# Performance work log

Measured on AMD Instinct MI355X. Metric: run time of the kernel, lower is better.

Reference implementation:

```python
import jax, jax.numpy as jnp
import numpy as np

N = 1_000_000          # total nodes (atoms)
F = 32                 # node feature dim
K = 16                 # kernels per degree
DEG_COUNTS = [200_000, 300_000, 300_000, 200_000]  # focal nodes per degree 1..4
EPS = 1e-8


def _unit(a):
    # L2-normalize along last axis (CosineSimilarity semantics)
    return a / (jnp.linalg.norm(a, axis=-1, keepdims=True) + EPS)


def setup_inputs() -> dict:
    key = jax.random.key(0)
    ks = jax.random.split(key, 16)
    x = jax.random.normal(ks[0], (N, F), dtype=jnp.float32)
    # selected indices: disjoint partition of all nodes by degree (a permutation)
    perm = jax.random.permutation(ks[1], N)
    sels, off = [], 0
    for c in DEG_COUNTS:
        sels.append(perm[off:off + c].astype(jnp.int64))
        off += c
    inp = {"x": x}
    for d in range(1, 5):
        inp[f"selected_index_deg{d}"] = sels[d - 1]
        inp[f"nei_index_deg{d}"] = jax.random.randint(
            ks[1 + d], (d * DEG_COUNTS[d - 1],), 0, N).astype(jnp.int64)
        inp[f"W_focal{d}"] = jax.random.normal(ks[7 + d], (K, F), dtype=jnp.float32)
        inp[f"W_nei{d}"] = jax.random.normal(ks[11 + d], (K, d, F), dtype=jnp.float32)
    return inp


def _degree_score(x, sel, nei, Wf, Wn, deg):
    # gather receptive field for this degree group
    x_focal = _unit(x[sel])                         # (Nd, F)
    x_nei = _unit(x[nei].reshape(-1, deg, F))       # (Nd, deg, F)
    sc_f = _unit(Wf) @ x_focal.T                    # (K, Nd) cosine vs focal kernel
    sc_n = jnp.einsum('kdf,ndf->kn', _unit(Wn), x_nei) / deg  # mean neighbor cosine
    return sc_f + sc_n                              # (K, Nd)


def reference(x,
              W_focal1, W_nei1, W_focal2, W_nei2,
              W_focal3, W_nei3, W_focal4, W_nei4,
              selected_index_deg1, selected_index_deg2,
              selected_index_deg3, selected_index_deg4,
              nei_index_deg1, nei_index_deg2,
              nei_index_deg3, nei_index_deg4):
    sels = [selected_index_deg1, selected_index_deg2,
            selected_index_deg3, selected_index_deg4]
    neis = [nei_index_deg1, nei_index_deg2, nei_index_deg3, nei_index_deg4]
    Wfs = [W_focal1, W_focal2, W_focal3, W_focal4]
    Wns = [W_nei1, W_nei2, W_nei3, W_nei4]

    out = jnp.zeros((4 * K, N), dtype=x.dtype)  # the `zeros` score matrix
    row, col = 0, 0
    for d in range(1, 5):
        sc = _degree_score(x, sels[d - 1], neis[d - 1], Wfs[d - 1], Wns[d - 1], d)
        nd = sels[d - 1].shape[0]
        out = out.at[row:row + K, col:col + nd].set(sc)
        row += K
        col += nd
    # reorder columns back to original node order (get_reorder_index -> sort)
    order = jnp.argsort(jnp.concatenate(sels))
    return out[:, order].T  # (N, 4*K)
```

## Files before the change

### kernel.cpp

```cpp
#include <hip/hip_runtime.h>
#include <math.h>

#define F 32
#define K 16
#define EPSN 1e-8f
#define NPB 512


typedef _Float16 half8 __attribute__((ext_vector_type(8)));
typedef float f32x4  __attribute__((ext_vector_type(4)));
typedef int   i32x2  __attribute__((ext_vector_type(2)));
typedef int   i32x4  __attribute__((ext_vector_type(4)));

#define VMWAIT(N) do { asm volatile("s_waitcnt vmcnt(%0)" :: "n"(N) : "memory"); \
                       __builtin_amdgcn_sched_barrier(0); } while (0)

__device__ __forceinline__ void gpair(f32x4& a, f32x4& b, const float* x,
                                      unsigned row, int kq) {
    const unsigned off = row * 128u + (unsigned)kq * 32u;
    asm volatile("global_load_dwordx4 %0, %1, %2"
                 : "=&v"(a) : "v"(off), "s"(x) : "memory");
    asm volatile("global_load_dwordx4 %0, %1, %2 offset:16"
                 : "=&v"(b) : "v"(off), "s"(x) : "memory");
}

__device__ __forceinline__ void gstore(float* out, unsigned off, f32x4 v) {
    asm volatile("global_store_dwordx4 %0, %1, %2"
                 :: "v"(off), "v"(v), "s"(out) : "memory");
}

template<int DEG> struct Idx;
template<> struct Idx<1> { int node; int n0;
    __device__ __forceinline__ int nb(int) const { return n0; } };
template<> struct Idx<2> { int node; i32x2 nn;
    __device__ __forceinline__ int nb(int j) const { return nn[j]; } };
template<> struct Idx<3> { int node; i32x2 nn; int n2;
    __device__ __forceinline__ int nb(int j) const { return j < 2 ? nn[j] : n2; } };
template<> struct Idx<4> { int node; i32x4 nn;
    __device__ __forceinline__ int nb(int j) const { return nn[j]; } };

template<int DEG>
__device__ __forceinline__ void load_idx(Idx<DEG>& d, const int* sel,
                                         const int* nei, int ic) {
    const unsigned so = (unsigned)ic << 2;
    asm volatile("global_load_dword %0, %1, %2"
                 : "=&v"(d.node) : "v"(so), "s"(sel) : "memory");
    const unsigned no = (unsigned)(ic * DEG) << 2;
    if constexpr (DEG == 1)
        asm volatile("global_load_dword %0, %1, %2"
                     : "=&v"(d.n0) : "v"(no), "s"(nei) : "memory");
    else if constexpr (DEG == 2)
        asm volatile("global_load_dwordx2 %0, %1, %2"
                     : "=&v"(d.nn) : "v"(no), "s"(nei) : "memory");
    else if constexpr (DEG == 3) {
        asm volatile("global_load_dwordx2 %0, %1, %2"
                     : "=&v"(d.nn) : "v"(no), "s"(nei) : "memory");
        asm volatile("global_load_dword %0, %1, %2 offset:8"
                     : "=&v"(d.n2) : "v"(no), "s"(nei) : "memory");
    } else
        asm volatile("global_load_dwordx4 %0, %1, %2"
                     : "=&v"(d.nn) : "v"(no), "s"(nei) : "memory");
}

template<int DEG>
__device__ __forceinline__ f32x4 slab_compute(f32x4 a, f32x4 b, f32x4 acc,
                                              const _Float16* sWh,
                                              const _Float16* sWl,
                                              int lane, int r) {
    float ss = a[0]*a[0] + a[1]*a[1] + a[2]*a[2] + a[3]*a[3]
             + b[0]*b[0] + b[1]*b[1] + b[2]*b[2] + b[3]*b[3];
    ss += __shfl_xor(ss, 16);
    ss += __shfl_xor(ss, 32);
    float sc = 1.f / (sqrtf(ss) + EPSN);
    if (r > 0) sc *= (1.f / (float)DEG);
    const float f0 = a[0]*sc, f1 = a[1]*sc, f2 = a[2]*sc, f3 = a[3]*sc;
    const float f4 = b[0]*sc, f5 = b[1]*sc, f6 = b[2]*sc, f7 = b[3]*sc;
    half8 bh, bl;
    bh[0]=(_Float16)f0; bl[0]=(_Float16)(f0-(float)bh[0]);
    bh[1]=(_Float16)f1; bl[1]=(_Float16)(f1-(float)bh[1]);
    bh[2]=(_Float16)f2; bl[2]=(_Float16)(f2-(float)bh[2]);
    bh[3]=(_Float16)f3; bl[3]=(_Float16)(f3-(float)bh[3]);
    bh[4]=(_Float16)f4; bl[4]=(_Float16)(f4-(float)bh[4]);
    bh[5]=(_Float16)f5; bl[5]=(_Float16)(f5-(float)bh[5]);
    bh[6]=(_Float16)f6; bl[6]=(_Float16)(f6-(float)bh[6]);
    bh[7]=(_Float16)f7; bl[7]=(_Float16)(f7-(float)bh[7]);
    const int aoff = r * 512 + lane * 8;
    const half8 ah = *(const half8*)(sWh + aoff);
    const half8 al = *(const half8*)(sWl + aoff);
    acc = __builtin_amdgcn_mfma_f32_16x16x32_f16(ah, bh, acc, 0, 0, 0);
    acc = __builtin_amdgcn_mfma_f32_16x16x32_f16(ah, bl, acc, 0, 0, 0);
    acc = __builtin_amdgcn_mfma_f32_16x16x32_f16(al, bh, acc, 0, 0, 0);
    return acc;
}

template<int DEG>
__device__ __forceinline__ void process_deg(const float* __restrict__ x,
                                            const int*   __restrict__ sel,
                                            const int*   __restrict__ nei,
                                            const float* __restrict__ Wf,
                                            const float* __restrict__ Wn,
                                            float* __restrict__ out,
                                            int nd, int i0,
                                            _Float16* sWh, _Float16* sWl)
{
    constexpr int R  = DEG + 1;
    constexpr int H  = (DEG <= 2) ? 1 : 2;
    constexpr int C0 = 2 * H;
    constexpr int C1 = 2 * (R - H);
    constexpr int NI = (DEG == 3) ? 3 : 2;
    constexpr int KB = C1 + NI;
    constexpr int KD = C0;
    constexpr int NW = K * R;
    constexpr int ITERS = NPB / 64;
    const int tid = threadIdx.x;

    if (tid < NW) {
        const float* src = (tid < K) ? (Wf + tid * F) : (Wn + (tid - K) * F);
        float ss = 0.f;
        #pragma unroll
        for (int f = 0; f < F; ++f) { const float t = src[f]; ss += t * t; }
        const float sc = 1.f / (sqrtf(ss) + EPSN);
        const int t = tid - K;
        const int r = (tid < K) ? 0   : (1 + t % DEG);
        const int k = (tid < K) ? tid : (t / DEG);
        #pragma unroll
        for (int f = 0; f < F; ++f) {
            const float wv = src[f] * sc;
            const _Float16 hi = (_Float16)wv;
            const _Float16 lo = (_Float16)(wv - (float)hi);
            const int off = r * 512 + (k + 16 * (f >> 3)) * 8 + (f & 7);
            sWh[off] = hi; sWl[off] = lo;
        }
    }
    __syncthreads();

    const int lane = tid & 63;
    const int wv   = tid >> 6;
    const int jcol = lane & 15;
    const int kq   = lane >> 4;
    const int i0w  = i0 + wv * 16 + jcol;

    f32x4 g0[2 * H], g1[2 * (R - H)];
    const f32x4 zed = {0.f, 0.f, 0.f, 0.f};

    Idx<DEG> ix, iy;
    { const int ic = (i0w < nd) ? i0w : (nd - 1);
      load_idx<DEG>(ix, sel, nei, ic); }
    { const int i1 = i0w + 64; const int ic = (i1 < nd) ? i1 : (nd - 1);
      load_idx<DEG>(iy, sel, nei, ic); }
    VMWAIT(NI);
    #pragma unroll
    for (int r = 0; r < H; ++r)
        gpair(g0[2*r], g0[2*r+1], x,
              (unsigned)((r == 0) ? ix.node : ix.nb(r-1)), kq);

#define ITER(T, XC, YN)                                                        \
    {                                                                          \
        const int nodeT = XC.node;                                             \
        _Pragma("unroll")                                                      \
        for (int r = H; r < R; ++r)                        \
            gpair(g1[2*(r-H)], g1[2*(r-H)+1], x, (unsigned)XC.nb(r-1), kq);    \
        { const int ii = i0w + ((T) + 2) * 64;         \
          load_idx<DEG>(XC, sel, nei, (ii < nd) ? ii : (nd - 1)); }            \
        VMWAIT(KB);                            \
        f32x4 acc = {0.f, 0.f, 0.f, 0.f};                                      \
        _Pragma("unroll")                                                      \
        for (int r = 0; r < H; ++r)                                            \
            acc = slab_compute<DEG>(g0[2*r], g0[2*r+1], acc, sWh, sWl, lane, r);\
        _Pragma("unroll")                                                      \
        for (int r = 0; r < H; ++r)                      \
            gpair(g0[2*r], g0[2*r+1], x,                                       \
                  (unsigned)((r == 0) ? YN.node : YN.nb(r-1)), kq);            \
        VMWAIT(KD);                                      \
        _Pragma("unroll")                                                      \
        for (int r = H; r < R; ++r)                                            \
            acc = slab_compute<DEG>(g1[2*(r-H)], g1[2*(r-H)+1], acc,           \
                                    sWh, sWl, lane, r);                        \
        if (i0w + (T) * 64 < nd) {                           \
            const unsigned ob = (unsigned)nodeT * 256u + (unsigned)kq * 16u;   \
            _Pragma("unroll")                                                  \
            for (int b = 0; b < 4; ++b)                                        \
                gstore(out, ob + (unsigned)b * 64u,                            \
                       (b == DEG - 1) ? acc : zed);                            \
        }                                                                      \
    }

    #pragma unroll 1
    for (int tp = 0; tp < ITERS; tp += 2) {
        ITER(tp,     ix, iy);
        ITER(tp + 1, iy, ix);
    }
#undef ITER
    VMWAIT(0);
}

struct Args {
    const float* x;
    const int*   sel[4];
    const int*   nei[4];
    const float* Wf[4];
    const float* Wn[4];
    int nd[4];
    int bcum[4];
};

__global__ __launch_bounds__(256, 2)
void fused_kernel(Args a, float* __restrict__ out)
{
    __shared__ __align__(16) _Float16 sWh[5 * 512];
    __shared__ __align__(16) _Float16 sWl[5 * 512];
    const int bid = blockIdx.x;

    if (bid < a.bcum[0]) {
        process_deg<1>(a.x, a.sel[0], a.nei[0], a.Wf[0], a.Wn[0], out,
                       a.nd[0], bid * NPB, sWh, sWl);
    } else if (bid < a.bcum[1]) {
        process_deg<2>(a.x, a.sel[1], a.nei[1], a.Wf[1], a.Wn[1], out,
                       a.nd[1], (bid - a.bcum[0]) * NPB, sWh, sWl);
    } else if (bid < a.bcum[2]) {
        process_deg<3>(a.x, a.sel[2], a.nei[2], a.Wf[2], a.Wn[2], out,
                       a.nd[2], (bid - a.bcum[1]) * NPB, sWh, sWl);
    } else {
        process_deg<4>(a.x, a.sel[3], a.nei[3], a.Wf[3], a.Wn[3], out,
                       a.nd[3], (bid - a.bcum[2]) * NPB, sWh, sWl);
    }
}

extern "C" void kernel_launch(void* const* d_in, const int* in_sizes, int n_in,
                              void* d_out, int out_size, void* d_ws, size_t ws_size,
                              hipStream_t stream)
{
    Args a;
    a.x = (const float*)d_in[0];
    for (int d = 0; d < 4; ++d) {
        a.sel[d] = (const int*)  d_in[1 + 4 * d];
        a.nei[d] = (const int*)  d_in[2 + 4 * d];
        a.Wf[d]  = (const float*)d_in[3 + 4 * d];
        a.Wn[d]  = (const float*)d_in[4 + 4 * d];
        a.nd[d]  = in_sizes[1 + 4 * d];
    }
    int cum = 0;
    for (int d = 0; d < 4; ++d) {
        cum += (a.nd[d] + NPB - 1) / NPB;
        a.bcum[d] = cum;
    }
    float* out = (float*)d_out;
    fused_kernel<<<cum, 256, 0, stream>>>(a, out);
}
```

Measured before the change: 447.7 us.

## Prenormalize x into an fp16 workspace copy and halve gather width

A new pre-pass kernel L2-normalizes every row of x once and stores it as fp16 in the workspace. The fused kernel then gathers 64-byte fp16 rows instead of 128-byte fp32 rows, and runs two MFMAs per slab instead of three because the activation low part is dropped. The 1/deg factor moves into the weight preparation. In exchange there is an extra full pass over x (read 128 MB, write 64 MB), and activations lose the fp16 error-compensation term, which reduces accuracy. A fallback path keeps the old fp32 approach when the workspace is too small.

Result: slower. 463.0 us (+3.4%).

```diff
diff --git a/kernel.cpp b/kernel.cpp
--- a/kernel.cpp
+++ b/kernel.cpp
@@ -5,6 +5,7 @@
 #define K 16
 #define EPSN 1e-8f
 #define NPB 512
+#define NPB_FB 256
 
 
 typedef _Float16 half8 __attribute__((ext_vector_type(8)));
@@ -15,13 +16,35 @@
 #define VMWAIT(N) do { asm volatile("s_waitcnt vmcnt(%0)" :: "n"(N) : "memory"); \
                        __builtin_amdgcn_sched_barrier(0); } while (0)
 
-__device__ __forceinline__ void gpair(f32x4& a, f32x4& b, const float* x,
-                                      unsigned row, int kq) {
-    const unsigned off = row * 128u + (unsigned)kq * 32u;
+__global__ __launch_bounds__(256)
+void norm_x_kernel(const float* __restrict__ x, _Float16* __restrict__ xh,
+                   int nrows)
+{
+    const int t   = blockIdx.x * 256 + threadIdx.x;
+    const int row = t >> 2;
+    const int p   = t & 3;
+    if (row >= nrows) return;
+    const float* xr = x + (size_t)row * F + p * 8;
+    const float4 a0 = *(const float4*)xr;
+    const float4 a1 = *(const float4*)(xr + 4);
+    float ss = a0.x*a0.x + a0.y*a0.y + a0.z*a0.z + a0.w*a0.w
+             + a1.x*a1.x + a1.y*a1.y + a1.z*a1.z + a1.w*a1.w;
+    ss += __shfl_xor(ss, 1);
+    ss += __shfl_xor(ss, 2);
+    const float sc = 1.f / (sqrtf(ss) + EPSN);
+    half8 h;
+    h[0] = (_Float16)(a0.x * sc); h[1] = (_Float16)(a0.y * sc);
+    h[2] = (_Float16)(a0.z * sc); h[3] = (_Float16)(a0.w * sc);
+    h[4] = (_Float16)(a1.x * sc); h[5] = (_Float16)(a1.y * sc);
+    h[6] = (_Float16)(a1.z * sc); h[7] = (_Float16)(a1.w * sc);
+    *(half8*)(xh + (size_t)row * F + p * 8) = h;
+}
+
+__device__ __forceinline__ void gload16(half8& d, const _Float16* xh,
+                                        unsigned row, int kq) {
+    const unsigned off = row * 64u + (unsigned)kq * 16u;
     asm volatile("global_load_dwordx4 %0, %1, %2"
-                 : "=&v"(a) : "v"(off), "s"(x) : "memory");
-    asm volatile("global_load_dwordx4 %0, %1, %2 offset:16"
-                 : "=&v"(b) : "v"(off), "s"(x) : "memory");
+                 : "=&v"(d) : "v"(off), "s"(xh) : "memory");
 }
 
 __device__ __forceinline__ void gstore(float* out, unsigned off, f32x4 v) {
@@ -62,39 +85,20 @@
                      : "=&v"(d.nn) : "v"(no), "s"(nei) : "memory");
 }
 
-template<int DEG>
-__device__ __forceinline__ f32x4 slab_compute(f32x4 a, f32x4 b, f32x4 acc,
-                                              const _Float16* sWh,
-                                              const _Float16* sWl,
-                                              int lane, int r) {
-    float ss = a[0]*a[0] + a[1]*a[1] + a[2]*a[2] + a[3]*a[3]
-             + b[0]*b[0] + b[1]*b[1] + b[2]*b[2] + b[3]*b[3];
-    ss += __shfl_xor(ss, 16);
-    ss += __shfl_xor(ss, 32);
-    float sc = 1.f / (sqrtf(ss) + EPSN);
-    if (r > 0) sc *= (1.f / (float)DEG);
-    const float f0 = a[0]*sc, f1 = a[1]*sc, f2 = a[2]*sc, f3 = a[3]*sc;
-    const float f4 = b[0]*sc, f5 = b[1]*sc, f6 = b[2]*sc, f7 = b[3]*sc;
-    half8 bh, bl;
-    bh[0]=(_Float16)f0; bl[0]=(_Float16)(f0-(float)bh[0]);
-    bh[1]=(_Float16)f1; bl[1]=(_Float16)(f1-(float)bh[1]);
-    bh[2]=(_Float16)f2; bl[2]=(_Float16)(f2-(float)bh[2]);
-    bh[3]=(_Float16)f3; bl[3]=(_Float16)(f3-(float)bh[3]);
-    bh[4]=(_Float16)f4; bl[4]=(_Float16)(f4-(float)bh[4]);
-    bh[5]=(_Float16)f5; bl[5]=(_Float16)(f5-(float)bh[5]);
-    bh[6]=(_Float16)f6; bl[6]=(_Float16)(f6-(float)bh[6]);
-    bh[7]=(_Float16)f7; bl[7]=(_Float16)(f7-(float)bh[7]);
+__device__ __forceinline__ f32x4 slab2(half8 b, f32x4 acc,
+                                       const _Float16* sWh,
+                                       const _Float16* sWl,
+                                       int lane, int r) {
     const int aoff = r * 512 + lane * 8;
     const half8 ah = *(const half8*)(sWh + aoff);
     const half8 al = *(const half8*)(sWl + aoff);
-    acc = __builtin_amdgcn_mfma_f32_16x16x32_f16(ah, bh, acc, 0, 0, 0);
-    acc = __builtin_amdgcn_mfma_f32_16x16x32_f16(ah, bl, acc, 0, 0, 0);
-    acc = __builtin_amdgcn_mfma_f32_16x16x32_f16(al, bh, acc, 0, 0, 0);
+    acc = __builtin_amdgcn_mfma_f32_16x16x32_f16(ah, b, acc, 0, 0, 0);
+    acc = __builtin_amdgcn_mfma_f32_16x16x32_f16(al, b, acc, 0, 0, 0);
     return acc;
 }
 
 template<int DEG>
-__device__ __forceinline__ void process_deg(const float* __restrict__ x,
+__device__ __forceinline__ void process_deg(const _Float16* __restrict__ xh,
                                             const int*   __restrict__ sel,
                                             const int*   __restrict__ nei,
                                             const float* __restrict__ Wf,
@@ -105,8 +109,8 @@
 {
     constexpr int R  = DEG + 1;
     constexpr int H  = (DEG <= 2) ? 1 : 2;
-    constexpr int C0 = 2 * H;
-    constexpr int C1 = 2 * (R - H);
+    constexpr int C0 = H;
+    constexpr int C1 = R - H;
     constexpr int NI = (DEG == 3) ? 3 : 2;
     constexpr int KB = C1 + NI;
     constexpr int KD = C0;
@@ -119,10 +123,11 @@
         float ss = 0.f;
         #pragma unroll
         for (int f = 0; f < F; ++f) { const float t = src[f]; ss += t * t; }
-        const float sc = 1.f / (sqrtf(ss) + EPSN);
         const int t = tid - K;
         const int r = (tid < K) ? 0   : (1 + t % DEG);
         const int k = (tid < K) ? tid : (t / DEG);
+        const float sc = (1.f / (sqrtf(ss) + EPSN))
+                       * ((r == 0) ? 1.f : 1.f / (float)DEG);
         #pragma unroll
         for (int f = 0; f < F; ++f) {
             const float wv = src[f] * sc;
@@ -140,7 +145,7 @@
     const int kq   = lane >> 4;
     const int i0w  = i0 + wv * 16 + jcol;
 
-    f32x4 g0[2 * H], g1[2 * (R - H)];
+    half8 g0[H], g1[R - H];
     const f32x4 zed = {0.f, 0.f, 0.f, 0.f};
 
     Idx<DEG> ix, iy;
@@ -151,31 +156,29 @@
     VMWAIT(NI);
     #pragma unroll
     for (int r = 0; r < H; ++r)
-        gpair(g0[2*r], g0[2*r+1], x,
-              (unsigned)((r == 0) ? ix.node : ix.nb(r-1)), kq);
+        gload16(g0[r], xh, (unsigned)((r == 0) ? ix.node : ix.nb(r-1)), kq);
 
 #define ITER(T, XC, YN)                                                        \
     {                                                                          \
         const int nodeT = XC.node;                                             \
         _Pragma("unroll")                                                      \
         for (int r = H; r < R; ++r)                        \
-            gpair(g1[2*(r-H)], g1[2*(r-H)+1], x, (unsigned)XC.nb(r-1), kq);    \
+            gload16(g1[r - H], xh, (unsigned)XC.nb(r-1), kq);                  \
         { const int ii = i0w + ((T) + 2) * 64;         \
           load_idx<DEG>(XC, sel, nei, (ii < nd) ? ii : (nd - 1)); }            \
         VMWAIT(KB);                            \
         f32x4 acc = {0.f, 0.f, 0.f, 0.f};                                      \
         _Pragma("unroll")                                                      \
         for (int r = 0; r < H; ++r)                                            \
-            acc = slab_compute<DEG>(g0[2*r], g0[2*r+1], acc, sWh, sWl, lane, r);\
+            acc = slab2(g0[r], acc, sWh, sWl, lane, r);                        \
         _Pragma("unroll")                                                      \
         for (int r = 0; r < H; ++r)                      \
-            gpair(g0[2*r], g0[2*r+1], x,                                       \
-                  (unsigned)((r == 0) ? YN.node : YN.nb(r-1)), kq);            \
+            gload16(g0[r], xh,                                                 \
+                    (unsigned)((r == 0) ? YN.node : YN.nb(r-1)), kq);          \
         VMWAIT(KD);                                      \
         _Pragma("unroll")                                                      \
         for (int r = H; r < R; ++r)                                            \
-            acc = slab_compute<DEG>(g1[2*(r-H)], g1[2*(r-H)+1], acc,           \
-                                    sWh, sWl, lane, r);                        \
+            acc = slab2(g1[r - H], acc, sWh, sWl, lane, r);                    \
         if (i0w + (T) * 64 < nd) {                           \
             const unsigned ob = (unsigned)nodeT * 256u + (unsigned)kq * 16u;   \
             _Pragma("unroll")                                                  \
@@ -195,6 +198,128 @@
 }
 
 struct Args {
+    const _Float16* xh;
+    const int*   sel[4];
+    const int*   nei[4];
+    const float* Wf[4];
+    const float* Wn[4];
+    int nd[4];
+    int bcum[4];
+};
+
+__global__ __launch_bounds__(256, 2)
+void fused_kernel(Args a, float* __restrict__ out)
+{
+    __shared__ __align__(16) _Float16 sWh[5 * 512];
+    __shared__ __align__(16) _Float16 sWl[5 * 512];
+    const int bid = blockIdx.x;
+
+    if (bid < a.bcum[0]) {
+        process_deg<1>(a.xh, a.sel[0], a.nei[0], a.Wf[0], a.Wn[0], out,
+                       a.nd[0], bid * NPB, sWh, sWl);
+    } else if (bid < a.bcum[1]) {
+        process_deg<2>(a.xh, a.sel[1], a.nei[1], a.Wf[1], a.Wn[1], out,
+                       a.nd[1], (bid - a.bcum[0]) * NPB, sWh, sWl);
+    } else if (bid < a.bcum[2]) {
+        process_deg<3>(a.xh, a.sel[2], a.nei[2], a.Wf[2], a.Wn[2], out,
+                       a.nd[2], (bid - a.bcum[1]) * NPB, sWh, sWl);
+    } else {
+        process_deg<4>(a.xh, a.sel[3], a.nei[3], a.Wf[3], a.Wn[3], out,
+                       a.nd[3], (bid - a.bcum[2]) * NPB, sWh, sWl);
+    }
+}
+
+template<int DEG>
+__device__ __forceinline__ void process_fb(const float* __restrict__ x,
+                                           const int*   __restrict__ sel,
+                                           const int*   __restrict__ nei,
+                                           const float* __restrict__ Wf,
+                                           const float* __restrict__ Wn,
+                                           float* __restrict__ out,
+                                           int nd, int i0,
+                                           _Float16* sWh, _Float16* sWl)
+{
+    constexpr int R  = 1 + DEG;
+    constexpr int NW = K * R;
+    const int tid = threadIdx.x;
+    if (tid < NW) {
+        const float* src = (tid < K) ? (Wf + tid * F) : (Wn + (tid - K) * F);
+        float ss = 0.f;
+        #pragma unroll
+        for (int f = 0; f < F; ++f) { const float t = src[f]; ss += t * t; }
+        const float sc = 1.f / (sqrtf(ss) + EPSN);
+        const int t = tid - K;
+        const int r = (tid < K) ? 0   : (1 + t % DEG);
+        const int k = (tid < K) ? tid : (t / DEG);
+        #pragma unroll
+        for (int f = 0; f < F; ++f) {
+            const float wv = src[f] * sc;
+            const _Float16 hi = (_Float16)wv;
+            const _Float16 lo = (_Float16)(wv - (float)hi);
+            const int off = r * 512 + (k + 16 * (f >> 3)) * 8 + (f & 7);
+            sWh[off] = hi; sWl[off] = lo;
+        }
+    }
+    __syncthreads();
+
+    const int lane = tid & 63, wv = tid >> 6;
+    const int jcol = lane & 15, kq = lane >> 4;
+    const float invdeg = 1.f / (float)DEG;
+
+    #pragma unroll 1
+    for (int it = 0; it < NPB_FB / 64; ++it) {
+        int i = i0 + it * 64 + wv * 16 + jcol;
+        const bool valid = (i < nd);
+        if (!valid) i = nd - 1;
+        const int node = sel[i];
+        int nn[DEG];
+        #pragma unroll
+        for (int j = 0; j < DEG; ++j) nn[j] = nei[i * DEG + j];
+        f32x4 acc = {0.f, 0.f, 0.f, 0.f};
+        #pragma unroll
+        for (int r = 0; r < R; ++r) {
+            const unsigned row = (unsigned)((r == 0) ? node : nn[r - 1]);
+            const float* xr = x + row * (unsigned)F + kq * 8;
+            const float4 a0 = *(const float4*)(xr);
+            const float4 a1 = *(const float4*)(xr + 4);
+            float ss = a0.x*a0.x + a0.y*a0.y + a0.z*a0.z + a0.w*a0.w
+                     + a1.x*a1.x + a1.y*a1.y + a1.z*a1.z + a1.w*a1.w;
+            ss += __shfl_xor(ss, 16);
+            ss += __shfl_xor(ss, 32);
+            float sc = 1.f / (sqrtf(ss) + EPSN);
+            if (r > 0) sc *= invdeg;
+            const float f0 = a0.x*sc, f1 = a0.y*sc, f2 = a0.z*sc, f3 = a0.w*sc;
+            const float f4 = a1.x*sc, f5 = a1.y*sc, f6 = a1.z*sc, f7 = a1.w*sc;
+            half8 bh, bl;
+            bh[0]=(_Float16)f0; bl[0]=(_Float16)(f0-(float)bh[0]);
+            bh[1]=(_Float16)f1; bl[1]=(_Float16)(f1-(float)bh[1]);
+            bh[2]=(_Float16)f2; bl[2]=(_Float16)(f2-(float)bh[2]);
+            bh[3]=(_Float16)f3; bl[3]=(_Float16)(f3-(float)bh[3]);
+            bh[4]=(_Float16)f4; bl[4]=(_Float16)(f4-(float)bh[4]);
+            bh[5]=(_Float16)f5; bl[5]=(_Float16)(f5-(float)bh[5]);
+            bh[6]=(_Float16)f6; bl[6]=(_Float16)(f6-(float)bh[6]);
+            bh[7]=(_Float16)f7; bl[7]=(_Float16)(f7-(float)bh[7]);
+            const int aoff = r * 512 + lane * 8;
+            const half8 ah = *(const half8*)(sWh + aoff);
+            const half8 al = *(const half8*)(sWl + aoff);
+            acc = __builtin_amdgcn_mfma_f32_16x16x32_f16(ah, bh, acc, 0, 0, 0);
+            acc = __builtin_amdgcn_mfma_f32_16x16x32_f16(ah, bl, acc, 0, 0, 0);
+            acc = __builtin_amdgcn_mfma_f32_16x16x32_f16(al, bh, acc, 0, 0, 0);
+        }
+        if (valid) {
+            float* orow = out + (size_t)node * (4 * K);
+            #pragma unroll
+            for (int b = 0; b < 4; ++b) {
+                float4 vst = make_float4(0.f, 0.f, 0.f, 0.f);
+                if (b == DEG - 1)
+                    vst = make_float4(acc[0], acc[1], acc[2], acc[3]);
+                *(float4*)(orow + (b * 4 + kq) * 4) = vst;
+            }
+        }
+    }
+}
+
+struct ArgsFb {
     const float* x;
     const int*   sel[4];
     const int*   nei[4];
@@ -204,25 +329,24 @@
     int bcum[4];
 };
 
-__global__ __launch_bounds__(256, 2)
-void fused_kernel(Args a, float* __restrict__ out)
+__global__ __launch_bounds__(256)
+void fused_kernel_fb(ArgsFb a, float* __restrict__ out)
 {
     __shared__ __align__(16) _Float16 sWh[5 * 512];
     __shared__ __align__(16) _Float16 sWl[5 * 512];
     const int bid = blockIdx.x;
-
     if (bid < a.bcum[0]) {
-        process_deg<1>(a.x, a.sel[0], a.nei[0], a.Wf[0], a.Wn[0], out,
-                       a.nd[0], bid * NPB, sWh, sWl);
+        process_fb<1>(a.x, a.sel[0], a.nei[0], a.Wf[0], a.Wn[0], out,
+                      a.nd[0], bid * NPB_FB, sWh, sWl);
     } else if (bid < a.bcum[1]) {
-        process_deg<2>(a.x, a.sel[1], a.nei[1], a.Wf[1], a.Wn[1], out,
-                       a.nd[1], (bid - a.bcum[0]) * NPB, sWh, sWl);
+        process_fb<2>(a.x, a.sel[1], a.nei[1], a.Wf[1], a.Wn[1], out,
+                      a.nd[1], (bid - a.bcum[0]) * NPB_FB, sWh, sWl);
     } else if (bid < a.bcum[2]) {
-        process_deg<3>(a.x, a.sel[2], a.nei[2], a.Wf[2], a.Wn[2], out,
-                       a.nd[2], (bid - a.bcum[1]) * NPB, sWh, sWl);
+        process_fb<3>(a.x, a.sel[2], a.nei[2], a.Wf[2], a.Wn[2], out,
+                      a.nd[2], (bid - a.bcum[1]) * NPB_FB, sWh, sWl);
     } else {
-        process_deg<4>(a.x, a.sel[3], a.nei[3], a.Wf[3], a.Wn[3], out,
-                       a.nd[3], (bid - a.bcum[2]) * NPB, sWh, sWl);
+        process_fb<4>(a.x, a.sel[3], a.nei[3], a.Wf[3], a.Wn[3], out,
+                      a.nd[3], (bid - a.bcum[2]) * NPB_FB, sWh, sWl);
     }
 }
 
@@ -230,20 +354,42 @@
                               void* d_out, int out_size, void* d_ws, size_t ws_size,
                               hipStream_t stream)
 {
-    Args a;
-    a.x = (const float*)d_in[0];
-    for (int d = 0; d < 4; ++d) {
-        a.sel[d] = (const int*)  d_in[1 + 4 * d];
-        a.nei[d] = (const int*)  d_in[2 + 4 * d];
-        a.Wf[d]  = (const float*)d_in[3 + 4 * d];
-        a.Wn[d]  = (const float*)d_in[4 + 4 * d];
-        a.nd[d]  = in_sizes[1 + 4 * d];
-    }
-    int cum = 0;
-    for (int d = 0; d < 4; ++d) {
-        cum += (a.nd[d] + NPB - 1) / NPB;
-        a.bcum[d] = cum;
-    }
+    const float* xp = (const float*)d_in[0];
+    const int nrows = in_sizes[0] / F;
+    const size_t need = (size_t)nrows * F * sizeof(_Float16);
     float* out = (float*)d_out;
-    fused_kernel<<<cum, 256, 0, stream>>>(a, out);
-}
+
+    if (d_ws != nullptr && ws_size >= need) {
+        _Float16* xh = (_Float16*)d_ws;
+        const int pre_blocks = (nrows * 4 + 255) / 256;
+        norm_x_kernel<<<pre_blocks, 256, 0, stream>>>(xp, xh, nrows);
+
+        Args a;
+        a.xh = xh;
+        int cum = 0;
+        for (int d = 0; d < 4; ++d) {
+            a.sel[d] = (const int*)  d_in[1 + 4 * d];
+            a.nei[d] = (const int*)  d_in[2 + 4 * d];
+            a.Wf[d]  = (const float*)d_in[3 + 4 * d];
+            a.Wn[d]  = (const float*)d_in[4 + 4 * d];
+            a.nd[d]  = in_sizes[1 + 4 * d];
+            cum += (a.nd[d] + NPB - 1) / NPB;
+            a.bcum[d] = cum;
+        }
+        fused_kernel<<<cum, 256, 0, stream>>>(a, out);
+    } else {
+        ArgsFb a;
+        a.x = xp;
+        int cum = 0;
+        for (int d = 0; d < 4; ++d) {
+            a.sel[d] = (const int*)  d_in[1 + 4 * d];
+            a.nei[d] = (const int*)  d_in[2 + 4 * d];
+            a.Wf[d]  = (const float*)d_in[3 + 4 * d];
+            a.Wn[d]  = (const float*)d_in[4 + 4 * d];
+            a.nd[d]  = in_sizes[1 + 4 * d];
+            cum += (a.nd[d] + NPB_FB - 1) / NPB_FB;
+            a.bcum[d] = cum;
+        }
+        fused_kernel_fb<<<cum, 256, 0, stream>>>(a, out);
+    }
+}
```
